# Performance work log

Measured on AMD Instinct MI355X. Metric: run time of the kernel, lower is better.

Reference implementation:

```python
import jax, jax.numpy as jnp
import numpy as np
from jax import lax

K = 512   # codebook size
D = 32    # latent dim == encoder out channels
DN = ('NCHW', 'OIHW', 'NCHW')


def _conv(x, w, b, stride):
    y = lax.conv_general_dilated(x, w, (stride, stride), ((1, 1), (1, 1)),
                                 dimension_numbers=DN)
    return y + b[None, :, None, None]


def _deconv(x, w, b):
    # torch ConvTranspose2d(k=4, s=2, p=1); weight layout (in, out, kh, kw).
    # Equivalent: conv with lhs_dilation=2, pad k-1-p = 2, spatially flipped,
    # in/out-swapped kernel.
    rhs = jnp.transpose(jnp.flip(w, (2, 3)), (1, 0, 2, 3))
    y = lax.conv_general_dilated(x, rhs, (1, 1), ((2, 2), (2, 2)),
                                 lhs_dilation=(2, 2), dimension_numbers=DN)
    return y + b[None, :, None, None]


def _forward(imgs, w1, b1, w2, b2, codebook, dw1, db1, dw2, db2):
    # Encoder
    h = jax.nn.relu(_conv(imgs, w1, b1, 2))
    z_e = jax.nn.relu(_conv(h, w2, b2, 2))          # (B, 32, H/4, W/4)
    # Vector quantize
    z = jnp.transpose(z_e, (0, 2, 3, 1))            # (B, h, w, D)
    flat = z.reshape(-1, D)                          # (N, D)
    dist = (jnp.sum(flat * flat, axis=1, keepdims=True)
            + jnp.sum(codebook * codebook, axis=1)
            - 2.0 * flat @ codebook.T)               # (N, K)
    q = jnp.argmin(dist, axis=1)                     # (N,)
    z_q = codebook[q].reshape(z.shape)               # gather == one-hot matmul
    codebook_loss = jnp.mean((lax.stop_gradient(z_q) - z) ** 2)
    commit_loss = jnp.mean((z_q - lax.stop_gradient(z)) ** 2)
    vq_loss = codebook_loss + commit_loss
    z_q_st = z + lax.stop_gradient(z_q - z)          # straight-through
    encoded = jnp.transpose(z_q_st, (0, 3, 1, 2))    # (B, 32, h, w)
    # Decoder
    d = jax.nn.relu(_deconv(encoded, dw1, db1))
    decoded = jax.nn.relu(_deconv(d, dw2, db2))
    return encoded, decoded, vq_loss


def setup_inputs() -> dict:
    key = jax.random.key(0)
    ks = jax.random.split(key, 8)

    def w_init(k, shape):
        fan_in = shape[1] * shape[2] * shape[3]
        bound = 1.0 / np.sqrt(fan_in)
        return jax.random.uniform(k, shape, jnp.float32, -bound, bound)

    imgs = jax.random.normal(ks[0], (32, 3, 256, 256), jnp.float32)
    w1 = w_init(ks[1], (16, 3, 4, 4));  b1 = jnp.zeros((16,), jnp.float32)
    w2 = w_init(ks[2], (32, 16, 4, 4)); b2 = jnp.zeros((32,), jnp.float32)
    # decoder ConvTranspose2d weights, torch layout (in, out, kh, kw)
    dw1 = w_init(ks[3], (32, 16, 4, 4)); db1 = jnp.zeros((16,), jnp.float32)
    dw2 = w_init(ks[4], (16, 3, 4, 4));  db2 = jnp.zeros((3,), jnp.float32)
    codebook = jax.random.uniform(ks[5], (K, D), jnp.float32, -1.0 / K, 1.0 / K)
    return dict(imgs=imgs, w1=w1, b1=b1, w2=w2, b2=b2, codebook=codebook,
                dw1=dw1, db1=db1, dw2=dw2, db2=db2)


def reference(imgs, w1, b1, w2, b2, codebook, dw1, db1, dw2, db2):
    return _forward(imgs, w1, b1, w2, b2, codebook, dw1, db1, dw2, db2)
```

## Files before the change

kernel.cpp:

```cpp
#include <hip/hip_runtime.h>
#include <float.h>

#pragma clang fp contract(off)

__device__ __forceinline__ float pw32(const float* p) {
  float r0 = p[0], r1 = p[1], r2 = p[2], r3 = p[3];
  float r4 = p[4], r5 = p[5], r6 = p[6], r7 = p[7];
  r0 += p[8];  r1 += p[9];  r2 += p[10]; r3 += p[11];
  r4 += p[12]; r5 += p[13]; r6 += p[14]; r7 += p[15];
  r0 += p[16]; r1 += p[17]; r2 += p[18]; r3 += p[19];
  r4 += p[20]; r5 += p[21]; r6 += p[22]; r7 += p[23];
  r0 += p[24]; r1 += p[25]; r2 += p[26]; r3 += p[27];
  r4 += p[28]; r5 += p[29]; r6 += p[30]; r7 += p[31];
  return ((r0 + r1) + (r2 + r3)) + ((r4 + r5) + (r6 + r7));
}

__global__ __launch_bounds__(256) void k_prep(
    const float* __restrict__ w1, const float* __restrict__ w2,
    const float* __restrict__ cb, const float* __restrict__ dw1,
    float* __restrict__ w1t, float* __restrict__ w2t,
    float* __restrict__ wd1t, float* __restrict__ bnG) {
  int t = threadIdx.x;
  for (int i = t; i < 8192; i += 256) {
    int tap = i >> 5, co = i & 31;
    w2t[i] = w2[co * 256 + tap];
  }
  for (int i = t; i < 768; i += 256) {
    int tap = i >> 4, co = i & 15;
    w1t[i] = w1[co * 48 + tap];
  }
  for (int i = t; i < 8192; i += 256) {
    int kk = i >> 9, ci = (i >> 4) & 31, co = i & 15;
    wd1t[i] = dw1[ci * 256 + co * 16 + kk];
  }
  for (int k = t; k < 512; k += 256) {
    float p[32];
    #pragma unroll
    for (int d = 0; d < 32; d++) { float c = cb[k * 32 + d]; p[d] = c * c; }
    bnG[k] = pw32(p);
  }
}

__global__ __launch_bounds__(256) void k_conv1(
    const float* __restrict__ img, const float* __restrict__ w1t,
    const float* __restrict__ b1, float* __restrict__ h1, int b0) {
  int idx = blockIdx.x * 256 + threadIdx.x;
  int x  = idx & 127;
  int y  = (idx >> 7) & 127;
  int bl = idx >> 14;
  const float* im = img + (long)(b0 + bl) * 196608;
  float acc[16];
  #pragma unroll
  for (int q = 0; q < 16; q++) acc[q] = 0.f;
  int iy0 = 2 * y - 1, ix0 = 2 * x - 1;
  for (int ci = 0; ci < 3; ci++) {
    const float* imc = im + ci * 65536;
    for (int r = 0; r < 4; r++) {
      int iy = iy0 + r;
      if ((unsigned)iy >= 256u) continue;
      const float* row = imc + iy * 256;
      for (int c = 0; c < 4; c++) {
        int ix = ix0 + c;
        float hv = ((unsigned)ix < 256u) ? row[ix] : 0.f;
        const float* wp = w1t + ((ci * 16 + r * 4 + c) << 4);
        #pragma unroll
        for (int co = 0; co < 16; co++)
          acc[co] = fmaf(hv, wp[co], acc[co]);
      }
    }
  }
  long hbase = (long)bl * 262144 + y * 128 + x;
  #pragma unroll
  for (int co = 0; co < 16; co++)
    h1[hbase + (long)co * 16384] = fmaxf(acc[co] + b1[co], 0.f);
}

__global__ __launch_bounds__(256, 3) void k_conv2z(
    const float* __restrict__ h1, const float* __restrict__ w2t,
    const float* __restrict__ b2, float* __restrict__ enct, int b0) {
  int t = threadIdx.x;
  int half = blockIdx.x & 1;
  int coff = half << 4;
  int ppix = (blockIdx.x >> 1) * 256 + t;
  int x  = ppix & 63;
  int y  = (ppix >> 6) & 63;
  int bl = ppix >> 12;
  int bg = b0 + bl;

  float z[16];
  #pragma unroll
  for (int q = 0; q < 16; q++) z[q] = 0.f;

  int iy0 = 2 * y - 1, ix0 = 2 * x - 1;
  for (int ci = 0; ci < 16; ci++) {
    long hbase = (long)bl * 262144 + (long)ci * 16384;
    for (int r = 0; r < 4; r++) {
      int iy = iy0 + r;
      if ((unsigned)iy >= 128u) continue;
      const float* hrow = h1 + hbase + (long)iy * 128;
      const float* wrow = w2t + ((ci * 16 + r * 4) << 5) + coff;
      for (int c = 0; c < 4; c++) {
        int ix = ix0 + c;
        float hv = ((unsigned)ix < 128u) ? hrow[ix] : 0.f;
        const float* wp = wrow + (c << 5);
        #pragma unroll
        for (int co = 0; co < 16; co++)
          z[co] = fmaf(hv, wp[co], z[co]);
      }
    }
  }
  float4* et4 = (float4*)(enct + ((long)bg * 4096 + y * 64 + x) * 32 + coff);
  #pragma unroll
  for (int d4 = 0; d4 < 4; d4++) {
    float4 v;
    v.x = fmaxf(z[d4 * 4 + 0] + b2[coff + d4 * 4 + 0], 0.f);
    v.y = fmaxf(z[d4 * 4 + 1] + b2[coff + d4 * 4 + 1], 0.f);
    v.z = fmaxf(z[d4 * 4 + 2] + b2[coff + d4 * 4 + 2], 0.f);
    v.w = fmaxf(z[d4 * 4 + 3] + b2[coff + d4 * 4 + 3], 0.f);
    et4[d4] = v;
  }
}

template <int W>
__device__ __forceinline__ double vq_epi(const float* cw, const float (&z)[32],
                                         float* __restrict__ enc, long ebase,
                                         float4* et4) {
  int d = W * 4;
  float f0 = cw[d + 0] - z[d + 0], e0 = z[d + 0] + f0;
  float f1 = cw[d + 1] - z[d + 1], e1 = z[d + 1] + f1;
  float f2 = cw[d + 2] - z[d + 2], e2 = z[d + 2] + f2;
  float f3 = cw[d + 3] - z[d + 3], e3 = z[d + 3] + f3;
  enc[ebase + (long)(d + 0) * 4096] = e0;
  enc[ebase + (long)(d + 1) * 4096] = e1;
  enc[ebase + (long)(d + 2) * 4096] = e2;
  enc[ebase + (long)(d + 3) * 4096] = e3;
  double ls = 0.0;
  ls += (double)f0 * (double)f0;
  ls += (double)f1 * (double)f1;
  ls += (double)f2 * (double)f2;
  ls += (double)f3 * (double)f3;
  float4 v; v.x = e0; v.y = e1; v.z = e2; v.w = e3;
  et4[W] = v;
  return ls;
}

__global__ __launch_bounds__(512) void k_vq(
    const float* __restrict__ cb, const float* __restrict__ bnG,
    float* __restrict__ enc, float* enct,
    double* __restrict__ partial, int b0) {
  __shared__ float sb[512];
  __shared__ int   sq[512];
  __shared__ double sls[8];
  int t = threadIdx.x, l = t & 63;
  int w = __builtin_amdgcn_readfirstlane(t >> 6);
  int yy = blockIdx.x & 63;
  int bl = blockIdx.x >> 6;
  int bg = b0 + bl;
  long pg = (long)bg * 4096 + yy * 64 + l;

  float z[32];
  const float4* z4 = (const float4*)(enct + pg * 32);
  #pragma unroll
  for (int i = 0; i < 8; i++) {
    float4 v = z4[i];
    z[i * 4 + 0] = v.x; z[i * 4 + 1] = v.y;
    z[i * 4 + 2] = v.z; z[i * 4 + 3] = v.w;
  }
  float pz[32];
  #pragma unroll
  for (int d = 0; d < 32; d++) pz[d] = z[d] * z[d];
  float a = pw32(pz);

  int kbase = w << 6;
  float best = FLT_MAX; int bq = kbase;
  for (int k = kbase; k < kbase + 64; k += 4) {
    const float* c0 = cb + (k << 5);
    float m0 = 0.f, m1 = 0.f, m2 = 0.f, m3 = 0.f;
    #pragma unroll
    for (int d = 0; d < 32; d++) {
      m0 = fmaf(z[d], c0[d],      m0);
      m1 = fmaf(z[d], c0[32 + d], m1);
      m2 = fmaf(z[d], c0[64 + d], m2);
      m3 = fmaf(z[d], c0[96 + d], m3);
    }
    float d0 = (a + bnG[k])     - 2.0f * m0;
    float d1 = (a + bnG[k + 1]) - 2.0f * m1;
    float d2 = (a + bnG[k + 2]) - 2.0f * m2;
    float d3 = (a + bnG[k + 3]) - 2.0f * m3;
    if (d0 < best) { best = d0; bq = k; }
    if (d1 < best) { best = d1; bq = k + 1; }
    if (d2 < best) { best = d2; bq = k + 2; }
    if (d3 < best) { best = d3; bq = k + 3; }
  }
  sb[t] = best; sq[t] = bq;
  __syncthreads();
  float gb = sb[l]; int gq = sq[l];
  #pragma unroll
  for (int ww = 1; ww < 8; ww++) {
    float ob = sb[(ww << 6) + l];
    int   oq = sq[(ww << 6) + l];
    if (ob < gb) { gb = ob; gq = oq; }
  }

  const float* cw = cb + (gq << 5);
  long ebase = (long)bg * 131072 + yy * 64 + l;
  float4* et4 = (float4*)(enct + pg * 32);
  double ls;
  if      (w == 0) ls = vq_epi<0>(cw, z, enc, ebase, et4);
  else if (w == 1) ls = vq_epi<1>(cw, z, enc, ebase, et4);
  else if (w == 2) ls = vq_epi<2>(cw, z, enc, ebase, et4);
  else if (w == 3) ls = vq_epi<3>(cw, z, enc, ebase, et4);
  else if (w == 4) ls = vq_epi<4>(cw, z, enc, ebase, et4);
  else if (w == 5) ls = vq_epi<5>(cw, z, enc, ebase, et4);
  else if (w == 6) ls = vq_epi<6>(cw, z, enc, ebase, et4);
  else             ls = vq_epi<7>(cw, z, enc, ebase, et4);

  #pragma unroll
  for (int off = 32; off > 0; off >>= 1)
    ls += __shfl_down(ls, off, 64);
  if (l == 0) sls[w] = ls;
  __syncthreads();
  if (t == 0) {
    double s = sls[0];
    #pragma unroll
    for (int ww = 1; ww < 8; ww++) s += sls[ww];
    partial[(long)b0 * 64 + blockIdx.x] = s;
  }
}

__global__ __launch_bounds__(256) void k_deconv1(
    const float* __restrict__ enct, const float* __restrict__ wd1t,
    const float* __restrict__ db1, float* __restrict__ d1t, int b0) {
  int t = threadIdx.x;
  int p = t & 63;
  int rowid = __builtin_amdgcn_readfirstlane(blockIdx.x * 4 + (t >> 6));
  int oy = rowid & 127;
  int bl = rowid >> 7;
  int bg = b0 + bl;
  float accE[16], accO[16];
  #pragma unroll
  for (int q = 0; q < 16; q++) { accE[q] = 0.f; accO[q] = 0.f; }
  int iyt = (oy + 1) >> 1;
  for (int sy = 0; sy < 2; sy++) {
    int iy = iyt - sy;
    if ((unsigned)iy >= 64u) continue;
    int ky = oy + 1 - 2 * iy;
    long rbase = ((long)bg * 4096 + iy * 64) * 32;
    for (int sx = 0; sx < 2; sx++) {
      int colA = p - sx;
      int colB = p + 1 - sx;
      const float* wE = wd1t + ((ky * 4 + 1 + 2 * sx) << 9);
      const float* wO = wd1t + ((ky * 4 + 2 * sx) << 9);
      float4 eA[8], eB[8];
      if ((unsigned)colA < 64u) {
        const float4* qa = (const float4*)(enct + rbase + (long)colA * 32);
        #pragma unroll
        for (int i = 0; i < 8; i++) eA[i] = qa[i];
      } else {
        #pragma unroll
        for (int i = 0; i < 8; i++) eA[i] = make_float4(0.f, 0.f, 0.f, 0.f);
      }
      if ((unsigned)colB < 64u) {
        const float4* qb = (const float4*)(enct + rbase + (long)colB * 32);
        #pragma unroll
        for (int i = 0; i < 8; i++) eB[i] = qb[i];
      } else {
        #pragma unroll
        for (int i = 0; i < 8; i++) eB[i] = make_float4(0.f, 0.f, 0.f, 0.f);
      }
      #pragma unroll
      for (int c4 = 0; c4 < 8; c4++) {
        float4 a4 = eA[c4], b4 = eB[c4];
        #pragma unroll
        for (int j = 0; j < 4; j++) {
          float ea = (j == 0) ? a4.x : (j == 1) ? a4.y : (j == 2) ? a4.z : a4.w;
          float eb = (j == 0) ? b4.x : (j == 1) ? b4.y : (j == 2) ? b4.z : b4.w;
          int ci = c4 * 4 + j;
          const float* we = wE + (ci << 4);
          const float* wo = wO + (ci << 4);
          #pragma unroll
          for (int co = 0; co < 16; co++) {
            accE[co] = fmaf(ea, we[co], accE[co]);
            accO[co] = fmaf(eb, wo[co], accO[co]);
          }
        }
      }
    }
  }
  long pg = (long)bl * 16384 + oy * 128 + 2 * p;
  float4* oE = (float4*)(d1t + pg * 16);
  float4* oO = (float4*)(d1t + (pg + 1) * 16);
  #pragma unroll
  for (int q = 0; q < 4; q++) {
    float4 vE, vO;
    vE.x = fmaxf(accE[q * 4 + 0] + db1[q * 4 + 0], 0.f);
    vE.y = fmaxf(accE[q * 4 + 1] + db1[q * 4 + 1], 0.f);
    vE.z = fmaxf(accE[q * 4 + 2] + db1[q * 4 + 2], 0.f);
    vE.w = fmaxf(accE[q * 4 + 3] + db1[q * 4 + 3], 0.f);
    vO.x = fmaxf(accO[q * 4 + 0] + db1[q * 4 + 0], 0.f);
    vO.y = fmaxf(accO[q * 4 + 1] + db1[q * 4 + 1], 0.f);
    vO.z = fmaxf(accO[q * 4 + 2] + db1[q * 4 + 2], 0.f);
    vO.w = fmaxf(accO[q * 4 + 3] + db1[q * 4 + 3], 0.f);
    oE[q] = vE;
    oO[q] = vO;
  }
}

__global__ __launch_bounds__(256) void k_deconv2(
    const float* __restrict__ d1t, const float* __restrict__ dw2,
    const float* __restrict__ db2, float* __restrict__ dec, int b0) {
  __shared__ float w[768];
  for (int i = threadIdx.x; i < 768; i += 256) {
    int ci = i & 15, kk = (i >> 4) & 15, co = i >> 8;
    w[i] = dw2[ci * 48 + co * 16 + kk];
  }
  __syncthreads();
  int idx = blockIdx.x * 256 + threadIdx.x;
  int ox = idx & 255;
  int oy = (idx >> 8) & 255;
  int bl = idx >> 16;
  int bg = b0 + bl;
  float acc[3] = {0.f, 0.f, 0.f};
  int iyt = (oy + 1) >> 1, ixt = (ox + 1) >> 1;
  for (int sy = 0; sy < 2; sy++) {
    int iy = iyt - sy;
    int ky = oy + 1 - 2 * iy;
    if ((unsigned)iy >= 128u || (unsigned)ky >= 4u) continue;
    for (int sx = 0; sx < 2; sx++) {
      int ix = ixt - sx;
      int kx = ox + 1 - 2 * ix;
      if ((unsigned)ix >= 128u || (unsigned)kx >= 4u) continue;
      const float4* dp4 =
          (const float4*)(d1t + ((long)bl * 16384 + iy * 128 + ix) * 16);
      float4 dv0 = dp4[0], dv1 = dp4[1], dv2 = dp4[2], dv3 = dp4[3];
      int kk4 = (ky * 4 + kx) << 4;
      #pragma unroll
      for (int co = 0; co < 3; co++) {
        const float4* wp4 = (const float4*)(w + (co << 8) + kk4);
        float4 w0 = wp4[0], w1 = wp4[1], w2 = wp4[2], w3 = wp4[3];
        float a = acc[co];
        a = fmaf(dv0.x, w0.x, a); a = fmaf(dv0.y, w0.y, a);
        a = fmaf(dv0.z, w0.z, a); a = fmaf(dv0.w, w0.w, a);
        a = fmaf(dv1.x, w1.x, a); a = fmaf(dv1.y, w1.y, a);
        a = fmaf(dv1.z, w1.z, a); a = fmaf(dv1.w, w1.w, a);
        a = fmaf(dv2.x, w2.x, a); a = fmaf(dv2.y, w2.y, a);
        a = fmaf(dv2.z, w2.z, a); a = fmaf(dv2.w, w2.w, a);
        a = fmaf(dv3.x, w3.x, a); a = fmaf(dv3.y, w3.y, a);
        a = fmaf(dv3.z, w3.z, a); a = fmaf(dv3.w, w3.w, a);
        acc[co] = a;
      }
    }
  }
  long obase = (long)bg * 196608 + oy * 256 + ox;
  #pragma unroll
  for (int co = 0; co < 3; co++)
    dec[obase + (long)co * 65536] = fmaxf(acc[co] + db2[co], 0.f);
}

__global__ __launch_bounds__(256) void k_loss(
    const double* __restrict__ partial, float* __restrict__ out) {
  __shared__ double r[256];
  int t = threadIdx.x;
  double s = 0.0;
  for (int i = t; i < 2048; i += 256) s += partial[i];
  r[t] = s;
  __syncthreads();
  for (int st = 128; st > 0; st >>= 1) {
    if (t < st) r[t] += r[t + st];
    __syncthreads();
  }
  if (t == 0) out[0] = (float)(2.0 * r[0] / 4194304.0);
}

extern "C" void kernel_launch(void* const* d_in, const int* in_sizes, int n_in,
                              void* d_out, int out_size, void* d_ws, size_t ws_size,
                              hipStream_t stream) {
  const float* imgs = (const float*)d_in[0];
  const float* w1   = (const float*)d_in[1];
  const float* b1   = (const float*)d_in[2];
  const float* w2   = (const float*)d_in[3];
  const float* b2   = (const float*)d_in[4];
  const float* cb   = (const float*)d_in[5];
  const float* dw1  = (const float*)d_in[6];
  const float* db1  = (const float*)d_in[7];
  const float* dw2  = (const float*)d_in[8];
  const float* db2  = (const float*)d_in[9];

  float* out = (float*)d_out;
  float* enc = out;
  float* dec = out + 4194304;
  float* vql = out + 10485760;
  float* enct = dec + 2097152;

  long ws = (long)ws_size;
  long top = (ws - 16384) & ~255L;
  double* partial = (double*)((char*)d_ws + top);
  top = (top - 2048) & ~255L;
  float* bnG = (float*)((char*)d_ws + top);
  top = (top - 32768) & ~255L;
  float* w2t = (float*)((char*)d_ws + top);
  top = (top - 3072) & ~255L;
  float* w1t = (float*)((char*)d_ws + top);
  top = (top - 32768) & ~255L;
  float* wd1t = (float*)((char*)d_ws + top);

  k_prep<<<1, 256, 0, stream>>>(w1, w2, cb, dw1, w1t, w2t, wd1t, bnG);

  int cc = 1;
  for (int c = 32; c >= 1; c >>= 1)
    if ((long)c * 1048576 <= top) { cc = c; break; }

  float* h1 = (float*)d_ws;
  for (int b0 = 0; b0 < 32; b0 += cc) {
    k_conv1<<<cc * 64, 256, 0, stream>>>(imgs, w1t, b1, h1, b0);
    k_conv2z<<<cc * 32, 256, 0, stream>>>(h1, w2t, b2, enct, b0);
    k_vq<<<cc * 64, 512, 0, stream>>>(cb, bnG, enc, enct, partial, b0);
  }

  float* d1t = (float*)d_ws;
  for (int b0 = 0; b0 < 32; b0 += cc) {
    k_deconv1<<<cc * 32, 256, 0, stream>>>(enct, wd1t, db1, d1t, b0);
    k_deconv2<<<cc * 256, 256, 0, stream>>>(d1t, dw2, db2, dec, b0);
  }

  k_loss<<<1, 256, 0, stream>>>(partial, vql);
}
```

Measured before the change: 362.0 us.

## Run VQ argmin with one wave per block over the full codebook

The VQ kernel moves from 8 waves per block, each scanning 64 codebook entries followed by a shared-memory argmin merge, to a single 64-thread wave that scans all 512 entries per pixel. This removes the LDS merge, both block barriers and the per-wave epilogue dispatch. In exchange each block does eight times more serial work and the grid has far fewer waves in flight, which lowers parallelism and latency hiding for the codebook loads. Tie-breaking stays sequential in k, so the selected index is unchanged.

```diff
diff --git a/kernel.cpp b/kernel.cpp
--- a/kernel.cpp
+++ b/kernel.cpp
@@ -121,38 +121,11 @@
   }
 }
 
-template <int W>
-__device__ __forceinline__ double vq_epi(const float* cw, const float (&z)[32],
-                                         float* __restrict__ enc, long ebase,
-                                         float4* et4) {
-  int d = W * 4;
-  float f0 = cw[d + 0] - z[d + 0], e0 = z[d + 0] + f0;
-  float f1 = cw[d + 1] - z[d + 1], e1 = z[d + 1] + f1;
-  float f2 = cw[d + 2] - z[d + 2], e2 = z[d + 2] + f2;
-  float f3 = cw[d + 3] - z[d + 3], e3 = z[d + 3] + f3;
-  enc[ebase + (long)(d + 0) * 4096] = e0;
-  enc[ebase + (long)(d + 1) * 4096] = e1;
-  enc[ebase + (long)(d + 2) * 4096] = e2;
-  enc[ebase + (long)(d + 3) * 4096] = e3;
-  double ls = 0.0;
-  ls += (double)f0 * (double)f0;
-  ls += (double)f1 * (double)f1;
-  ls += (double)f2 * (double)f2;
-  ls += (double)f3 * (double)f3;
-  float4 v; v.x = e0; v.y = e1; v.z = e2; v.w = e3;
-  et4[W] = v;
-  return ls;
-}
-
-__global__ __launch_bounds__(512) void k_vq(
+__global__ __launch_bounds__(64) void k_vq(
     const float* __restrict__ cb, const float* __restrict__ bnG,
     float* __restrict__ enc, float* enct,
     double* __restrict__ partial, int b0) {
-  __shared__ float sb[512];
-  __shared__ int   sq[512];
-  __shared__ double sls[8];
-  int t = threadIdx.x, l = t & 63;
-  int w = __builtin_amdgcn_readfirstlane(t >> 6);
+  int l = threadIdx.x;
   int yy = blockIdx.x & 63;
   int bl = blockIdx.x >> 6;
   int bg = b0 + bl;
@@ -171,9 +144,8 @@
   for (int d = 0; d < 32; d++) pz[d] = z[d] * z[d];
   float a = pw32(pz);
 
-  int kbase = w << 6;
-  float best = FLT_MAX; int bq = kbase;
-  for (int k = kbase; k < kbase + 64; k += 4) {
+  float best = FLT_MAX; int bq = 0;
+  for (int k = 0; k < 512; k += 4) {
     const float* c0 = cb + (k << 5);
     float m0 = 0.f, m1 = 0.f, m2 = 0.f, m3 = 0.f;
     #pragma unroll
@@ -192,40 +164,33 @@
     if (d2 < best) { best = d2; bq = k + 2; }
     if (d3 < best) { best = d3; bq = k + 3; }
   }
-  sb[t] = best; sq[t] = bq;
-  __syncthreads();
-  float gb = sb[l]; int gq = sq[l];
-  #pragma unroll
-  for (int ww = 1; ww < 8; ww++) {
-    float ob = sb[(ww << 6) + l];
-    int   oq = sq[(ww << 6) + l];
-    if (ob < gb) { gb = ob; gq = oq; }
-  }
-
-  const float* cw = cb + (gq << 5);
+
+  const float* cw = cb + (bq << 5);
   long ebase = (long)bg * 131072 + yy * 64 + l;
   float4* et4 = (float4*)(enct + pg * 32);
-  double ls;
-  if      (w == 0) ls = vq_epi<0>(cw, z, enc, ebase, et4);
-  else if (w == 1) ls = vq_epi<1>(cw, z, enc, ebase, et4);
-  else if (w == 2) ls = vq_epi<2>(cw, z, enc, ebase, et4);
-  else if (w == 3) ls = vq_epi<3>(cw, z, enc, ebase, et4);
-  else if (w == 4) ls = vq_epi<4>(cw, z, enc, ebase, et4);
-  else if (w == 5) ls = vq_epi<5>(cw, z, enc, ebase, et4);
-  else if (w == 6) ls = vq_epi<6>(cw, z, enc, ebase, et4);
-  else             ls = vq_epi<7>(cw, z, enc, ebase, et4);
-
+  double ls = 0.0;
+  #pragma unroll
+  for (int d4 = 0; d4 < 8; d4++) {
+    int d = d4 * 4;
+    float f0 = cw[d + 0] - z[d + 0], e0 = z[d + 0] + f0;
+    float f1 = cw[d + 1] - z[d + 1], e1 = z[d + 1] + f1;
+    float f2 = cw[d + 2] - z[d + 2], e2 = z[d + 2] + f2;
+    float f3 = cw[d + 3] - z[d + 3], e3 = z[d + 3] + f3;
+    enc[ebase + (long)(d + 0) * 4096] = e0;
+    enc[ebase + (long)(d + 1) * 4096] = e1;
+    enc[ebase + (long)(d + 2) * 4096] = e2;
+    enc[ebase + (long)(d + 3) * 4096] = e3;
+    ls += (double)f0 * (double)f0;
+    ls += (double)f1 * (double)f1;
+    ls += (double)f2 * (double)f2;
+    ls += (double)f3 * (double)f3;
+    float4 v; v.x = e0; v.y = e1; v.z = e2; v.w = e3;
+    et4[d4] = v;
+  }
   #pragma unroll
   for (int off = 32; off > 0; off >>= 1)
     ls += __shfl_down(ls, off, 64);
-  if (l == 0) sls[w] = ls;
-  __syncthreads();
-  if (t == 0) {
-    double s = sls[0];
-    #pragma unroll
-    for (int ww = 1; ww < 8; ww++) s += sls[ww];
-    partial[(long)b0 * 64 + blockIdx.x] = s;
-  }
+  if (l == 0) partial[(long)b0 * 64 + blockIdx.x] = ls;
 }
 
 __global__ __launch_bounds__(256) void k_deconv1(
@@ -414,7 +379,7 @@
   for (int b0 = 0; b0 < 32; b0 += cc) {
     k_conv1<<<cc * 64, 256, 0, stream>>>(imgs, w1t, b1, h1, b0);
     k_conv2z<<<cc * 32, 256, 0, stream>>>(h1, w2t, b2, enct, b0);
-    k_vq<<<cc * 64, 512, 0, stream>>>(cb, bnG, enc, enct, partial, b0);
+    k_vq<<<cc * 64, 64, 0, stream>>>(cb, bnG, enc, enct, partial, b0);
   }
 
   float* d1t = (float*)d_ws;
```

Result: slower. 437.0 us (+20.7%).
